# Optimization experiments

Measured on AMD Instinct MI355X. Metric: run time of the kernel, lower is better.

The kernel has to match this reference:

```python
import jax, jax.numpy as jnp
import numpy as np

N_HEADS = 16
HIDDEN = 256
DIM = 4096
SEQ_LEN = 4096
BATCH = 8192
DECAY_CONSTANT = SEQ_LEN // 512  # = 8


def setup_inputs() -> dict:
    key = jax.random.key(0)
    ks = jax.random.split(key, 9)
    return {
        "x": jax.random.normal(ks[0], (BATCH, DIM), dtype=jnp.float32),
        "proj_w": jax.random.normal(ks[1], (N_HEADS, HIDDEN, DIM), dtype=jnp.float32) * 0.02,
        "proj_b": jax.random.normal(ks[2], (N_HEADS, HIDDEN), dtype=jnp.float32) * 0.02,
        "mix_w": jax.random.normal(ks[3], (N_HEADS, SEQ_LEN), dtype=jnp.float32) * 0.02 + 1.0,
        "mix_b": jax.random.normal(ks[4], (N_HEADS, SEQ_LEN), dtype=jnp.float32) * 0.02,
        "decay_value": jax.random.uniform(ks[5], (N_HEADS,), dtype=jnp.float32, minval=0.85, maxval=1.05),
        "cache": jax.random.normal(ks[6], (N_HEADS, BATCH, HIDDEN), dtype=jnp.float32),
        "out_w": jax.random.normal(ks[7], (DIM, DIM), dtype=jnp.float32) * 0.02,
        "out_b": jax.random.normal(ks[8], (DIM,), dtype=jnp.float32) * 0.02,
        "index": 1000,
    }


def reference(x, proj_w, proj_b, mix_w, mix_b, decay_value, cache, out_w, out_b, index):
    # Per-head projections: [h, b, k]
    proj = jnp.einsum("bd,hkd->hbk", x, proj_w) + proj_b[:, None, :]

    # Mixer params at the given sequence index (scalar per head)
    w = mix_w[:, index]          # [h]
    b = mix_b[:, index]          # [h]
    decay = jnp.clip(decay_value, 0.9, 1.0) ** (1.0 / DECAY_CONSTANT)  # [h]

    # First n_heads//2 heads are Col-style: out = w*x + w*decay*cache + b
    # Last  n_heads//2 heads are Row-style: out = w*x +   decay*cache + b
    is_col = jnp.arange(N_HEADS) < (N_HEADS // 2)
    cache_coef = jnp.where(is_col, w * decay, decay)  # [h]

    out = (w[:, None, None] * proj
           + cache_coef[:, None, None] * cache
           + b[:, None, None])  # [h, b, k]

    # Concatenate heads along feature axis -> [batch, n_heads*hidden] = [batch, dim]
    hidden = jnp.transpose(out, (1, 0, 2)).reshape(x.shape[0], N_HEADS * HIDDEN)

    return hidden @ out_w.T + out_b
```

## Files before the change

### kernel.cpp

```cpp
#include <hip/hip_runtime.h>
#include <hip/hip_bf16.h>

#define MROW 8192
#define DIMK 4096
#define NCOL 4096
#define HID  256
#define NH   16
#define SEQL 4096

#define BKT 32
#define NKT (DIMK / BKT)
#define SLOTB 32768
#define LDS_TOTAL (4 * SLOTB)

typedef __attribute__((ext_vector_type(8))) short short8;
typedef __attribute__((ext_vector_type(4))) float f32x4;

__device__ inline ushort f2bf(float f) {
  unsigned u = __float_as_uint(f);
  u += 0x7FFF + ((u >> 16) & 1);
  return (ushort)(u >> 16);
}

__device__ inline void gload16(const void* g, void* l) {
  __builtin_amdgcn_global_load_lds(
      (const __attribute__((address_space(1))) void*)g,
      (__attribute__((address_space(3))) void*)l, 16, 0, 0);
}

__global__ void cvt_f32_bf16(const float* __restrict__ s, ushort* __restrict__ d, long n8) {
  long stride = (long)gridDim.x * blockDim.x;
  for (long i = (long)blockIdx.x * blockDim.x + threadIdx.x; i < n8; i += stride) {
    const float4* s4 = (const float4*)(s + i * 8);
    float4 a = s4[0], b = s4[1];
    ushort r[8] = {f2bf(a.x), f2bf(a.y), f2bf(a.z), f2bf(a.w),
                   f2bf(b.x), f2bf(b.y), f2bf(b.z), f2bf(b.w)};
    *(uint4*)(d + i * 8) = *(const uint4*)r;
  }
}

__global__ void coef_kernel(const float* __restrict__ mix_w, const float* __restrict__ mix_b,
                            const float* __restrict__ decay_value, const float* __restrict__ proj_b,
                            const int* __restrict__ index_p,
                            float* __restrict__ wv, float* __restrict__ cc, float* __restrict__ pb2) {
  int n = blockIdx.x * blockDim.x + threadIdx.x;
  if (n >= NCOL) return;
  int h = n >> 8;
  int idx = *index_p;
  float w  = mix_w[h * SEQL + idx];
  float bb = mix_b[h * SEQL + idx];
  float dv = fminf(fmaxf(decay_value[h], 0.9f), 1.0f);
  float decay = powf(dv, 0.125f);
  float coef = (h < NH / 2) ? w * decay : decay;
  wv[n]  = w;
  cc[n]  = coef;
  pb2[n] = w * proj_b[n] + bb;
}

template <int EPI>
__global__ __launch_bounds__(1024, 4) void gemm256(
    const ushort* __restrict__ A, const ushort* __restrict__ B,
    float* __restrict__ outf, ushort* __restrict__ outh,
    const float* __restrict__ cache, const float* __restrict__ wv,
    const float* __restrict__ cc, const float* __restrict__ pb2,
    const float* __restrict__ outb) {
  extern __shared__ __align__(16) char smem[];

  const int tid  = threadIdx.x;
  const int lane = tid & 63;
  const int wid  = tid >> 6;
  const int wr = wid >> 2;
  const int wc = wid & 3;
  const int r16 = lane & 15;
  const int cq  = lane >> 4;

  const int bid = blockIdx.x;
  const int swz = (bid & 7) * 64 + (bid >> 3);
  const int bm = swz >> 4, bn = swz & 15;
  const int m0 = bm * 256, n0 = bn * 256;

  const ushort* Ag = A + (size_t)m0 * DIMK;
  const ushort* Bg = B + (size_t)n0 * DIMK;

  int aoff[4], boff[4];
#pragma unroll
  for (int i = 0; i < 4; ++i) {
    int arow = wr * 64 + i * 16 + r16;
    aoff[i] = arow * 64 + ((cq ^ ((arow >> 1) & 3)) << 4);
    int brow = wc * 64 + i * 16 + r16;
    boff[i] = 16384 + brow * 64 + ((cq ^ ((brow >> 1) & 3)) << 4);
  }

  const int soff = tid * 16;
  const int srow = soff >> 6;
  const int sgo  = srow * DIMK + ((((soff >> 4) & 3) ^ ((srow >> 1) & 3)) << 3);

  f32x4 acc[4][4] = {};

#pragma unroll
  for (int kt = 0; kt < 3; ++kt) {
    char* s = smem + kt * SLOTB;
    gload16(Ag + (size_t)sgo + kt * BKT, s + soff);
    gload16(Bg + (size_t)sgo + kt * BKT, s + 16384 + soff);
  }
  asm volatile("s_waitcnt vmcnt(4)" ::: "memory");
  __builtin_amdgcn_s_barrier();
  __builtin_amdgcn_sched_barrier(0);

  for (int kt = 0; kt < NKT; ++kt) {
    const char* cur = smem + (kt & 3) * SLOTB;

    short8 af[4], bf[4];
#pragma unroll
    for (int i = 0; i < 4; ++i) bf[i] = *(const short8*)(cur + boff[i]);
#pragma unroll
    for (int i = 0; i < 4; ++i) af[i] = *(const short8*)(cur + aoff[i]);

    if (kt < NKT - 3) {
      char* st = smem + ((kt + 3) & 3) * SLOTB;
      int k0 = (kt + 3) * BKT;
      gload16(Ag + (size_t)sgo + k0, st + soff);
      gload16(Bg + (size_t)sgo + k0, st + 16384 + soff);
    }

    __builtin_amdgcn_s_setprio(1);
#pragma unroll
    for (int mi = 0; mi < 4; ++mi)
#pragma unroll
      for (int ni = 0; ni < 4; ++ni)
        acc[mi][ni] = __builtin_amdgcn_mfma_f32_16x16x32_bf16(af[mi], bf[ni], acc[mi][ni], 0, 0, 0);
    __builtin_amdgcn_s_setprio(0);

    if (kt < NKT - 3)       asm volatile("s_waitcnt vmcnt(4)" ::: "memory");
    else if (kt == NKT - 3) asm volatile("s_waitcnt vmcnt(2)" ::: "memory");
    else if (kt == NKT - 2) asm volatile("s_waitcnt vmcnt(0)" ::: "memory");
    __builtin_amdgcn_s_barrier();
    __builtin_amdgcn_sched_barrier(0);
  }

  const int colb = n0 + wc * 64 + r16;
  const int rowb = m0 + wr * 64 + cq * 4;

  float wvv[4], ccv[4], pbv[4], obv[4];
#pragma unroll
  for (int ni = 0; ni < 4; ++ni) {
    int n = colb + ni * 16;
    if (EPI == 1) { wvv[ni] = wv[n]; ccv[ni] = cc[n]; pbv[ni] = pb2[n]; }
    else          { obv[ni] = outb[n]; }
  }

#pragma unroll
  for (int mi = 0; mi < 4; ++mi) {
#pragma unroll
    for (int ni = 0; ni < 4; ++ni) {
      f32x4 v = acc[mi][ni];
      int n = colb + ni * 16;
#pragma unroll
      for (int r = 0; r < 4; ++r) {
        int m = rowb + mi * 16 + r;
        if (EPI == 1) {
          int h = n >> 8, kq = n & 255;
          float val = wvv[ni] * v[r] + ccv[ni] * cache[((size_t)h * MROW + m) * HID + kq] + pbv[ni];
          outh[(size_t)m * NCOL + n] = f2bf(val);
        } else {
          outf[(size_t)m * NCOL + n] = v[r] + obv[ni];
        }
      }
    }
  }
}

extern "C" void kernel_launch(void* const* d_in, const int* in_sizes, int n_in,
                              void* d_out, int out_size, void* d_ws, size_t ws_size,
                              hipStream_t stream) {
  const float* x      = (const float*)d_in[0];
  const float* proj_w = (const float*)d_in[1];
  const float* proj_b = (const float*)d_in[2];
  const float* mix_w  = (const float*)d_in[3];
  const float* mix_b  = (const float*)d_in[4];
  const float* decay  = (const float*)d_in[5];
  const float* cache  = (const float*)d_in[6];
  const float* out_w  = (const float*)d_in[7];
  const float* out_b  = (const float*)d_in[8];
  const int*   index  = (const int*)d_in[9];

  char* ws = (char*)d_ws;
  ushort* xb  = (ushort*)ws;
  ushort* pwb = (ushort*)(ws + 67108864);
  ushort* owb = (ushort*)(ws + 100663296);
  ushort* hid = (ushort*)(ws + 134217728);
  float*  wv  = (float*)(ws + 201326592);
  float*  cc  = (float*)(ws + 201326592 + 16384);
  float*  pb2 = (float*)(ws + 201326592 + 32768);

  hipFuncSetAttribute((const void*)&gemm256<1>, hipFuncAttributeMaxDynamicSharedMemorySize, LDS_TOTAL);
  hipFuncSetAttribute((const void*)&gemm256<0>, hipFuncAttributeMaxDynamicSharedMemorySize, LDS_TOTAL);

  hipLaunchKernelGGL(cvt_f32_bf16, dim3(2048), dim3(256), 0, stream,
                     x, xb, (long)MROW * DIMK / 8);
  hipLaunchKernelGGL(cvt_f32_bf16, dim3(1024), dim3(256), 0, stream,
                     proj_w, pwb, (long)NCOL * DIMK / 8);
  hipLaunchKernelGGL(cvt_f32_bf16, dim3(1024), dim3(256), 0, stream,
                     out_w, owb, (long)NCOL * DIMK / 8);
  hipLaunchKernelGGL(coef_kernel, dim3(16), dim3(256), 0, stream,
                     mix_w, mix_b, decay, proj_b, index, wv, cc, pb2);

  hipLaunchKernelGGL((gemm256<1>), dim3((MROW / 256) * (NCOL / 256)), dim3(1024), LDS_TOTAL, stream,
                     xb, pwb, nullptr, hid, cache, wv, cc, pb2, nullptr);
  hipLaunchKernelGGL((gemm256<0>), dim3((MROW / 256) * (NCOL / 256)), dim3(1024), LDS_TOTAL, stream,
                     hid, owb, (float*)d_out, nullptr, nullptr, nullptr, nullptr, nullptr, out_b);
}
```

Measured before the change: 596.7 us.

## Use 512-thread blocks with 128x64 wave tiles and register-prefetched LDS fragments

Halves the threads per block from 1024 to 512, so each wave now computes a 128x64 output sub-tile (8x4 MFMA accumulators) instead of 64x64. Each thread issues two global-to-LDS loads per operand per stage to cover the same 256x256 block tile. The main loop is software-pipelined: the next k-step's A/B fragments are read from LDS into registers during the current step's MFMAs, and the A and B prefetch loads are split around the two MFMA halves. This cuts LDS reads per MFMA and overlaps LDS latency with compute, at the cost of higher register pressure and a shallower effective global prefetch depth.

```diff
diff --git a/kernel.cpp b/kernel.cpp
--- a/kernel.cpp
+++ b/kernel.cpp
@@ -58,7 +58,7 @@
 }
 
 template <int EPI>
-__global__ __launch_bounds__(1024, 4) void gemm256(
+__global__ __launch_bounds__(512, 2) void gemmp(
     const ushort* __restrict__ A, const ushort* __restrict__ B,
     float* __restrict__ outf, ushort* __restrict__ outh,
     const float* __restrict__ cache, const float* __restrict__ wv,
@@ -82,64 +82,102 @@
   const ushort* Ag = A + (size_t)m0 * DIMK;
   const ushort* Bg = B + (size_t)n0 * DIMK;
 
-  int aoff[4], boff[4];
+  int aoff[8], boff[4];
+#pragma unroll
+  for (int i = 0; i < 8; ++i) {
+    int arow = wr * 128 + i * 16 + r16;
+    aoff[i] = arow * 64 + ((cq ^ ((arow >> 1) & 3)) << 4);
+  }
 #pragma unroll
   for (int i = 0; i < 4; ++i) {
-    int arow = wr * 64 + i * 16 + r16;
-    aoff[i] = arow * 64 + ((cq ^ ((arow >> 1) & 3)) << 4);
     int brow = wc * 64 + i * 16 + r16;
     boff[i] = 16384 + brow * 64 + ((cq ^ ((brow >> 1) & 3)) << 4);
   }
 
-  const int soff = tid * 16;
-  const int srow = soff >> 6;
-  const int sgo  = srow * DIMK + ((((soff >> 4) & 3) ^ ((srow >> 1) & 3)) << 3);
-
-  f32x4 acc[4][4] = {};
+  int soff[2], sgo[2];
+#pragma unroll
+  for (int j = 0; j < 2; ++j) {
+    int off = j * 8192 + tid * 16;
+    int row = off >> 6;
+    soff[j] = off;
+    sgo[j]  = row * DIMK + ((((off >> 4) & 3) ^ ((row >> 1) & 3)) << 3);
+  }
+
+  f32x4 acc[8][4] = {};
 
 #pragma unroll
   for (int kt = 0; kt < 3; ++kt) {
     char* s = smem + kt * SLOTB;
-    gload16(Ag + (size_t)sgo + kt * BKT, s + soff);
-    gload16(Bg + (size_t)sgo + kt * BKT, s + 16384 + soff);
+#pragma unroll
+    for (int j = 0; j < 2; ++j) {
+      gload16(Ag + (size_t)sgo[j] + kt * BKT, s + soff[j]);
+      gload16(Bg + (size_t)sgo[j] + kt * BKT, s + 16384 + soff[j]);
+    }
   }
   asm volatile("s_waitcnt vmcnt(4)" ::: "memory");
   __builtin_amdgcn_s_barrier();
   __builtin_amdgcn_sched_barrier(0);
 
+  short8 blo[4], alo[4];
+#pragma unroll
+  for (int i = 0; i < 4; ++i) blo[i] = *(const short8*)(smem + boff[i]);
+#pragma unroll
+  for (int i = 0; i < 4; ++i) alo[i] = *(const short8*)(smem + aoff[i]);
+
   for (int kt = 0; kt < NKT; ++kt) {
     const char* cur = smem + (kt & 3) * SLOTB;
-
-    short8 af[4], bf[4];
-#pragma unroll
-    for (int i = 0; i < 4; ++i) bf[i] = *(const short8*)(cur + boff[i]);
-#pragma unroll
-    for (int i = 0; i < 4; ++i) af[i] = *(const short8*)(cur + aoff[i]);
-
-    if (kt < NKT - 3) {
-      char* st = smem + ((kt + 3) & 3) * SLOTB;
-      int k0 = (kt + 3) * BKT;
-      gload16(Ag + (size_t)sgo + k0, st + soff);
-      gload16(Bg + (size_t)sgo + k0, st + 16384 + soff);
-    }
-
+    const char* nxt = smem + ((kt + 1) & 3) * SLOTB;
+    char*       st  = smem + ((kt + 3) & 3) * SLOTB;
+    const bool  do_st = kt < NKT - 3;
+    const int   k3 = (kt + 3) * BKT;
+
+    short8 ahi[4];
+#pragma unroll
+    for (int i = 0; i < 4; ++i) ahi[i] = *(const short8*)(cur + aoff[4 + i]);
+    if (do_st) {
+      gload16(Ag + (size_t)sgo[0] + k3, st + soff[0]);
+      gload16(Ag + (size_t)sgo[1] + k3, st + soff[1]);
+    }
+    __builtin_amdgcn_sched_barrier(0);
     __builtin_amdgcn_s_setprio(1);
 #pragma unroll
     for (int mi = 0; mi < 4; ++mi)
 #pragma unroll
       for (int ni = 0; ni < 4; ++ni)
-        acc[mi][ni] = __builtin_amdgcn_mfma_f32_16x16x32_bf16(af[mi], bf[ni], acc[mi][ni], 0, 0, 0);
+        acc[mi][ni] = __builtin_amdgcn_mfma_f32_16x16x32_bf16(alo[mi], blo[ni], acc[mi][ni], 0, 0, 0);
     __builtin_amdgcn_s_setprio(0);
 
+    short8 bn[4], an[4];
+    if (kt < NKT - 1) {
+#pragma unroll
+      for (int i = 0; i < 4; ++i) bn[i] = *(const short8*)(nxt + boff[i]);
+#pragma unroll
+      for (int i = 0; i < 4; ++i) an[i] = *(const short8*)(nxt + aoff[i]);
+    }
+    if (do_st) {
+      gload16(Bg + (size_t)sgo[0] + k3, st + 16384 + soff[0]);
+      gload16(Bg + (size_t)sgo[1] + k3, st + 16384 + soff[1]);
+    }
+    __builtin_amdgcn_sched_barrier(0);
+    __builtin_amdgcn_s_setprio(1);
+#pragma unroll
+    for (int mi = 0; mi < 4; ++mi)
+#pragma unroll
+      for (int ni = 0; ni < 4; ++ni)
+        acc[4 + mi][ni] = __builtin_amdgcn_mfma_f32_16x16x32_bf16(ahi[mi], blo[ni], acc[4 + mi][ni], 0, 0, 0);
+    __builtin_amdgcn_s_setprio(0);
+
     if (kt < NKT - 3)       asm volatile("s_waitcnt vmcnt(4)" ::: "memory");
-    else if (kt == NKT - 3) asm volatile("s_waitcnt vmcnt(2)" ::: "memory");
-    else if (kt == NKT - 2) asm volatile("s_waitcnt vmcnt(0)" ::: "memory");
+    else if (kt == NKT - 3) asm volatile("s_waitcnt vmcnt(0)" ::: "memory");
     __builtin_amdgcn_s_barrier();
     __builtin_amdgcn_sched_barrier(0);
+
+#pragma unroll
+    for (int i = 0; i < 4; ++i) { blo[i] = bn[i]; alo[i] = an[i]; }
   }
 
   const int colb = n0 + wc * 64 + r16;
-  const int rowb = m0 + wr * 64 + cq * 4;
+  const int rowb = m0 + wr * 128 + cq * 4;
 
   float wvv[4], ccv[4], pbv[4], obv[4];
 #pragma unroll
@@ -150,14 +188,15 @@
   }
 
 #pragma unroll
-  for (int mi = 0; mi < 4; ++mi) {
+  for (int am = 0; am < 8; ++am) {
+    int mrow = rowb + am * 16;
 #pragma unroll
     for (int ni = 0; ni < 4; ++ni) {
-      f32x4 v = acc[mi][ni];
+      f32x4 v = acc[am][ni];
       int n = colb + ni * 16;
 #pragma unroll
       for (int r = 0; r < 4; ++r) {
-        int m = rowb + mi * 16 + r;
+        int m = mrow + r;
         if (EPI == 1) {
           int h = n >> 8, kq = n & 255;
           float val = wvv[ni] * v[r] + ccv[ni] * cache[((size_t)h * MROW + m) * HID + kq] + pbv[ni];
@@ -193,8 +232,8 @@
   float*  cc  = (float*)(ws + 201326592 + 16384);
   float*  pb2 = (float*)(ws + 201326592 + 32768);
 
-  hipFuncSetAttribute((const void*)&gemm256<1>, hipFuncAttributeMaxDynamicSharedMemorySize, LDS_TOTAL);
-  hipFuncSetAttribute((const void*)&gemm256<0>, hipFuncAttributeMaxDynamicSharedMemorySize, LDS_TOTAL);
+  hipFuncSetAttribute((const void*)&gemmp<1>, hipFuncAttributeMaxDynamicSharedMemorySize, LDS_TOTAL);
+  hipFuncSetAttribute((const void*)&gemmp<0>, hipFuncAttributeMaxDynamicSharedMemorySize, LDS_TOTAL);
 
   hipLaunchKernelGGL(cvt_f32_bf16, dim3(2048), dim3(256), 0, stream,
                      x, xb, (long)MROW * DIMK / 8);
@@ -205,8 +244,8 @@
   hipLaunchKernelGGL(coef_kernel, dim3(16), dim3(256), 0, stream,
                      mix_w, mix_b, decay, proj_b, index, wv, cc, pb2);
 
-  hipLaunchKernelGGL((gemm256<1>), dim3((MROW / 256) * (NCOL / 256)), dim3(1024), LDS_TOTAL, stream,
+  hipLaunchKernelGGL((gemmp<1>), dim3((MROW / 256) * (NCOL / 256)), dim3(512), LDS_TOTAL, stream,
                      xb, pwb, nullptr, hid, cache, wv, cc, pb2, nullptr);
-  hipLaunchKernelGGL((gemm256<0>), dim3((MROW / 256) * (NCOL / 256)), dim3(1024), LDS_TOTAL, stream,
+  hipLaunchKernelGGL((gemmp<0>), dim3((MROW / 256) * (NCOL / 256)), dim3(512), LDS_TOTAL, stream,
                      hid, owb, (float*)d_out, nullptr, nullptr, nullptr, nullptr, nullptr, out_b);
 }
```

Result: no change. 599.3 us (+0.4%).

## Restructure GEMM into 8-wave 256x256 tiles with BK=64 double-buffered ping-pong pipeline

Applied to the files above, without the earlier changes.

Replaces the 16-wave, 4-slot BK=32 GEMM with an 8-wave kernel where each wave computes a 128x64 sub-tile, using BK=64 and two 64KB LDS buffers. The main loop is split into four phases that interleave LDS fragment reads, global-to-LDS staging of the next tile, and MFMA bursts with barriers, in the style of a ping-pong schedule. The larger per-wave tile is meant to raise MFMA work per LDS read and cut barrier overhead per k-step. In exchange it doubles the accumulator registers per thread and adds more barriers per iteration, which could lower occupancy or cause stalls.

```diff
diff --git a/kernel.cpp b/kernel.cpp
--- a/kernel.cpp
+++ b/kernel.cpp
@@ -8,13 +8,16 @@
 #define NH   16
 #define SEQL 4096
 
-#define BKT 32
+#define BKT 64
 #define NKT (DIMK / BKT)
-#define SLOTB 32768
-#define LDS_TOTAL (4 * SLOTB)
+#define BUFB 65536
+#define LDS_TOTAL (2 * BUFB)
 
 typedef __attribute__((ext_vector_type(8))) short short8;
 typedef __attribute__((ext_vector_type(4))) float f32x4;
+
+#define LG0() do { asm volatile("s_waitcnt lgkmcnt(0)" ::: "memory"); \
+                   __builtin_amdgcn_sched_barrier(0); } while (0)
 
 __device__ inline ushort f2bf(float f) {
   unsigned u = __float_as_uint(f);
@@ -58,7 +61,7 @@
 }
 
 template <int EPI>
-__global__ __launch_bounds__(1024, 4) void gemm256(
+__global__ __launch_bounds__(512, 2) void gemmkp(
     const ushort* __restrict__ A, const ushort* __restrict__ B,
     float* __restrict__ outf, ushort* __restrict__ outh,
     const float* __restrict__ cache, const float* __restrict__ wv,
@@ -82,64 +85,85 @@
   const ushort* Ag = A + (size_t)m0 * DIMK;
   const ushort* Bg = B + (size_t)n0 * DIMK;
 
-  int aoff[4], boff[4];
-#pragma unroll
-  for (int i = 0; i < 4; ++i) {
-    int arow = wr * 64 + i * 16 + r16;
-    aoff[i] = arow * 64 + ((cq ^ ((arow >> 1) & 3)) << 4);
-    int brow = wc * 64 + i * 16 + r16;
-    boff[i] = 16384 + brow * 64 + ((cq ^ ((brow >> 1) & 3)) << 4);
-  }
-
-  const int soff = tid * 16;
-  const int srow = soff >> 6;
-  const int sgo  = srow * DIMK + ((((soff >> 4) & 3) ^ ((srow >> 1) & 3)) << 3);
-
-  f32x4 acc[4][4] = {};
-
-#pragma unroll
-  for (int kt = 0; kt < 3; ++kt) {
-    char* s = smem + kt * SLOTB;
-    gload16(Ag + (size_t)sgo + kt * BKT, s + soff);
-    gload16(Bg + (size_t)sgo + kt * BKT, s + 16384 + soff);
-  }
-  asm volatile("s_waitcnt vmcnt(4)" ::: "memory");
+  const int sx    = (cq ^ ((r16 >> 1) & 3)) << 4;
+  const int aBase = (wr * 128 + r16) * 64 + sx;
+  const int bBase = (wc * 64 + r16) * 64 + sx;
+
+  int ldst[2], sgo[2];
+#pragma unroll
+  for (int j = 0; j < 2; ++j) {
+    int off = j * 8192 + tid * 16;
+    int row = off >> 6;
+    ldst[j] = off;
+    sgo[j]  = row * DIMK + ((((off >> 4) & 3) ^ ((row >> 1) & 3)) << 3);
+  }
+
+  f32x4 acc[8][4] = {};
+  short8 af[4], bf[4];
+
+#define RD_B(ks) do { _Pragma("unroll") for (int n_ = 0; n_ < 4; ++n_)          \
+    bf[n_] = *(const short8*)(cur + 32768 + (ks)*16384 + bBase + n_*1024); } while (0)
+#define RD_A(ks, mh) do { _Pragma("unroll") for (int i_ = 0; i_ < 4; ++i_)      \
+    af[i_] = *(const short8*)(cur + (ks)*16384 + aBase + (mh)*4096 + i_*1024); } while (0)
+#define MM(mh) do {                                                             \
+    __builtin_amdgcn_s_setprio(1);                                              \
+    _Pragma("unroll") for (int i_ = 0; i_ < 4; ++i_)                            \
+      _Pragma("unroll") for (int n_ = 0; n_ < 4; ++n_)                          \
+        acc[(mh)*4+i_][n_] = __builtin_amdgcn_mfma_f32_16x16x32_bf16(           \
+            af[i_], bf[n_], acc[(mh)*4+i_][n_], 0, 0, 0);                       \
+    __builtin_amdgcn_s_setprio(0); } while (0)
+#define STG_A(ks, t, buf) do { _Pragma("unroll") for (int j_ = 0; j_ < 2; ++j_) \
+    gload16(Ag + (size_t)sgo[j_] + (size_t)(t)*BKT + (ks)*32,                   \
+            (buf) + (ks)*16384 + ldst[j_]); } while (0)
+#define STG_B(ks, t, buf) do { _Pragma("unroll") for (int j_ = 0; j_ < 2; ++j_) \
+    gload16(Bg + (size_t)sgo[j_] + (size_t)(t)*BKT + (ks)*32,                   \
+            (buf) + 32768 + (ks)*16384 + ldst[j_]); } while (0)
+
+  STG_A(0, 0, smem); STG_B(0, 0, smem); STG_A(1, 0, smem); STG_B(1, 0, smem);
+  asm volatile("s_waitcnt vmcnt(0)" ::: "memory");
   __builtin_amdgcn_s_barrier();
-  __builtin_amdgcn_sched_barrier(0);
 
   for (int kt = 0; kt < NKT; ++kt) {
-    const char* cur = smem + (kt & 3) * SLOTB;
-
-    short8 af[4], bf[4];
-#pragma unroll
-    for (int i = 0; i < 4; ++i) bf[i] = *(const short8*)(cur + boff[i]);
-#pragma unroll
-    for (int i = 0; i < 4; ++i) af[i] = *(const short8*)(cur + aoff[i]);
-
-    if (kt < NKT - 3) {
-      char* st = smem + ((kt + 3) & 3) * SLOTB;
-      int k0 = (kt + 3) * BKT;
-      gload16(Ag + (size_t)sgo + k0, st + soff);
-      gload16(Bg + (size_t)sgo + k0, st + 16384 + soff);
-    }
-
-    __builtin_amdgcn_s_setprio(1);
-#pragma unroll
-    for (int mi = 0; mi < 4; ++mi)
-#pragma unroll
-      for (int ni = 0; ni < 4; ++ni)
-        acc[mi][ni] = __builtin_amdgcn_mfma_f32_16x16x32_bf16(af[mi], bf[ni], acc[mi][ni], 0, 0, 0);
-    __builtin_amdgcn_s_setprio(0);
-
-    if (kt < NKT - 3)       asm volatile("s_waitcnt vmcnt(4)" ::: "memory");
-    else if (kt == NKT - 3) asm volatile("s_waitcnt vmcnt(2)" ::: "memory");
-    else if (kt == NKT - 2) asm volatile("s_waitcnt vmcnt(0)" ::: "memory");
-    __builtin_amdgcn_s_barrier();
-    __builtin_amdgcn_sched_barrier(0);
-  }
+    const char* cur = smem + (kt & 1) * BUFB;
+    char*       nxt = smem + ((kt + 1) & 1) * BUFB;
+    const bool  st   = (kt + 1) < NKT;
+    const bool  last = (kt == NKT - 1);
+
+    RD_B(0); RD_A(0, 0);
+    if (st) STG_A(0, kt + 1, nxt);
+    __builtin_amdgcn_s_barrier(); LG0();
+    MM(0);
+    __builtin_amdgcn_s_barrier();
+
+    RD_A(0, 1);
+    if (st) STG_B(0, kt + 1, nxt);
+    __builtin_amdgcn_s_barrier(); LG0();
+    MM(1);
+    if (last) asm volatile("s_waitcnt vmcnt(0)" ::: "memory");
+    else      asm volatile("s_waitcnt vmcnt(4)" ::: "memory");
+    __builtin_amdgcn_s_barrier();
+
+    RD_B(1); RD_A(1, 0);
+    if (st) STG_A(1, kt + 1, nxt);
+    __builtin_amdgcn_s_barrier(); LG0();
+    MM(0);
+    __builtin_amdgcn_s_barrier();
+
+    RD_A(1, 1);
+    if (st) STG_B(1, kt + 1, nxt);
+    __builtin_amdgcn_s_barrier(); LG0();
+    MM(1);
+    if (!last) asm volatile("s_waitcnt vmcnt(4)" ::: "memory");
+    __builtin_amdgcn_s_barrier();
+  }
+#undef RD_A
+#undef RD_B
+#undef MM
+#undef STG_A
+#undef STG_B
 
   const int colb = n0 + wc * 64 + r16;
-  const int rowb = m0 + wr * 64 + cq * 4;
+  const int rowb = m0 + wr * 128 + cq * 4;
 
   float wvv[4], ccv[4], pbv[4], obv[4];
 #pragma unroll
@@ -150,14 +174,15 @@
   }
 
 #pragma unroll
-  for (int mi = 0; mi < 4; ++mi) {
+  for (int am = 0; am < 8; ++am) {
+    int mrow = rowb + am * 16;
 #pragma unroll
     for (int ni = 0; ni < 4; ++ni) {
-      f32x4 v = acc[mi][ni];
+      f32x4 v = acc[am][ni];
       int n = colb + ni * 16;
 #pragma unroll
       for (int r = 0; r < 4; ++r) {
-        int m = rowb + mi * 16 + r;
+        int m = mrow + r;
         if (EPI == 1) {
           int h = n >> 8, kq = n & 255;
           float val = wvv[ni] * v[r] + ccv[ni] * cache[((size_t)h * MROW + m) * HID + kq] + pbv[ni];
@@ -193,8 +218,8 @@
   float*  cc  = (float*)(ws + 201326592 + 16384);
   float*  pb2 = (float*)(ws + 201326592 + 32768);
 
-  hipFuncSetAttribute((const void*)&gemm256<1>, hipFuncAttributeMaxDynamicSharedMemorySize, LDS_TOTAL);
-  hipFuncSetAttribute((const void*)&gemm256<0>, hipFuncAttributeMaxDynamicSharedMemorySize, LDS_TOTAL);
+  hipFuncSetAttribute((const void*)&gemmkp<1>, hipFuncAttributeMaxDynamicSharedMemorySize, LDS_TOTAL);
+  hipFuncSetAttribute((const void*)&gemmkp<0>, hipFuncAttributeMaxDynamicSharedMemorySize, LDS_TOTAL);
 
   hipLaunchKernelGGL(cvt_f32_bf16, dim3(2048), dim3(256), 0, stream,
                      x, xb, (long)MROW * DIMK / 8);
@@ -205,8 +230,10 @@
   hipLaunchKernelGGL(coef_kernel, dim3(16), dim3(256), 0, stream,
                      mix_w, mix_b, decay, proj_b, index, wv, cc, pb2);
 
-  hipLaunchKernelGGL((gemm256<1>), dim3((MROW / 256) * (NCOL / 256)), dim3(1024), LDS_TOTAL, stream,
+  const int grid = (MROW / 256) * (NCOL / 256);
+
+  hipLaunchKernelGGL((gemmkp<1>), dim3(grid), dim3(512), LDS_TOTAL, stream,
                      xb, pwb, nullptr, hid, cache, wv, cc, pb2, nullptr);
-  hipLaunchKernelGGL((gemm256<0>), dim3((MROW / 256) * (NCOL / 256)), dim3(1024), LDS_TOTAL, stream,
+  hipLaunchKernelGGL((gemmkp<0>), dim3(grid), dim3(512), LDS_TOTAL, stream,
                      hid, owb, (float*)d_out, nullptr, nullptr, nullptr, nullptr, nullptr, out_b);
 }
```

New measurement: 592.0 us. No clear change (-0.8%).
